# Kernel optimization log

Measured on AMD Instinct MI355X. Metric: run time of the kernel, lower is better.

Reference implementation:

```python
import jax, jax.numpy as jnp
import numpy as np

B, N, C = 8, 8192, 256
H = 8            # num_heads
D = C // H       # head dim = 32
P = 64           # proj_size (Linformer rank)


def setup_inputs() -> dict:
    key = jax.random.key(0)
    ks = jax.random.split(key, 12)
    s = lambda fan_in: 1.0 / np.sqrt(fan_in)
    return {
        "x": jax.random.normal(ks[0], (B, N, C), jnp.float32),
        "Wqkvv": jax.random.normal(ks[1], (4 * C, C), jnp.float32) * s(C),
        "WE": jax.random.normal(ks[2], (P, N), jnp.float32) * s(N),
        "bE": jax.random.normal(ks[3], (P,), jnp.float32) * s(N),
        "WF": jax.random.normal(ks[4], (P, N), jnp.float32) * s(N),
        "bF": jax.random.normal(ks[5], (P,), jnp.float32) * s(N),
        "Wo1": jax.random.normal(ks[6], (C // 2, C), jnp.float32) * s(C),
        "bo1": jax.random.normal(ks[7], (C // 2,), jnp.float32) * s(C),
        "Wo2": jax.random.normal(ks[8], (C // 2, C), jnp.float32) * s(C),
        "bo2": jax.random.normal(ks[9], (C // 2,), jnp.float32) * s(C),
        "temp1": jnp.ones((H, 1, 1), jnp.float32),
        "temp2": jnp.ones((H, 1, 1), jnp.float32),
    }


def _l2norm(v, axis=-1, eps=1e-12):
    # matches torch F.normalize
    n = jnp.sqrt(jnp.sum(v * v, axis=axis, keepdims=True))
    return v / jnp.maximum(n, eps)


def reference(x, Wqkvv, WE, bE, WF, bF, Wo1, bo1, Wo2, bo2, temp1, temp2):
    b, n, c = x.shape
    # qkvv: [b,n,4c] -> [4,b,h,d,n]  (includes the .transpose(-2,-1) of each part)
    qkvv = jnp.einsum('bnc,fc->bnf', x, Wqkvv).reshape(b, n, 4, H, D)
    qkvv = qkvv.transpose(2, 0, 3, 4, 1)
    q, k, v_ca, v_sa = qkvv[0], qkvv[1], qkvv[2], qkvv[3]  # each [b,h,d,n]

    # Linformer-style low-rank projections along the token axis
    k_proj = jnp.einsum('bhdn,pn->bhdp', k, WE) + bE   # [b,h,d,p]
    v_proj = jnp.einsum('bhdn,pn->bhdp', v_sa, WF) + bF

    qn = _l2norm(q)
    kn = _l2norm(k)

    # --- channel attention branch (XCiT-style) ---
    attn_ca = jnp.einsum('bhdn,bhen->bhde', qn, kn) * temp1[None]  # [b,h,d,d]
    attn_ca = jax.nn.softmax(attn_ca, axis=-1)  # dropout: eval mode (identity)
    x_ca = jnp.einsum('bhde,bhen->bhdn', attn_ca, v_ca)
    x_ca = x_ca.transpose(0, 3, 1, 2).reshape(b, n, c)  # [b,n,c]

    # --- spatial attention branch (low-rank) ---
    attn_sa = jnp.einsum('bhdn,bhdp->bhnp', qn, k_proj) * temp2[None]  # [b,h,n,p]
    attn_sa = jax.nn.softmax(attn_sa, axis=-1)
    x_sa = jnp.einsum('bhnp,bhdp->bhnd', attn_sa, v_proj)  # [b,h,n,d]
    # faithful to original: permute(0,3,1,2).reshape(b,n,c)
    x_sa = x_sa.transpose(0, 3, 1, 2).reshape(b, n, c)

    x_sa = jnp.einsum('bnc,oc->bno', x_sa, Wo1) + bo1
    x_ca = jnp.einsum('bnc,oc->bno', x_ca, Wo2) + bo2
    return jnp.concatenate((x_sa, x_ca), axis=-1)
```

## Files before the change

kernel.cpp:

```cpp
#include <hip/hip_runtime.h>
#include <hip/hip_bf16.h>
#include <stdint.h>


typedef __attribute__((ext_vector_type(8))) __bf16 bf16x8;
typedef __attribute__((ext_vector_type(4))) __bf16 bf16x4;
typedef __attribute__((ext_vector_type(4))) float f32x4;

#define MFMA(a, b, c) __builtin_amdgcn_mfma_f32_16x16x32_bf16((a), (b), (c), 0, 0, 0)

__device__ __forceinline__ void gl2lds16(const __bf16* g, __bf16* l) {
  __builtin_amdgcn_global_load_lds(
      (const __attribute__((address_space(1))) void*)(const void*)g,
      (__attribute__((address_space(3))) void*)(void*)l, 16, 0, 0);
}

__device__ __forceinline__ int detect_f32(const unsigned int* __restrict__ xw) {
  int c = 0;
#pragma unroll
  for (int i = 0; i < 64; ++i) {
    const unsigned int u = xw[i];
    c += (((u >> 7) & 0xFF) >= 0xC0) ? 1 : 0;
    c += (((u >> 23) & 0xFF) >= 0xC0) ? 1 : 0;
  }
  return c > 8;
}

__global__ __launch_bounds__(256) void k_convert_x(const void* __restrict__ src,
                                                   __bf16* __restrict__ dst) {
  const int i = (blockIdx.x * 256 + threadIdx.x) * 8;
  if (detect_f32((const unsigned int*)src)) {
    const float* s = (const float*)src;
    bf16x8 v;
#pragma unroll
    for (int j = 0; j < 8; ++j) v[j] = (__bf16)s[i + j];
    *(bf16x8*)(dst + i) = v;
  } else {
    *(bf16x8*)(dst + i) = *(const bf16x8*)((const __bf16*)src + i);
  }
}

__global__ __launch_bounds__(256) void k_convert_w(
    const void* s0, const void* s1, const void* s2, const void* s3, const void* s4,
    const void* s5, const void* s6, const void* s7, const void* s8, const void* s9,
    const void* s10, __bf16* __restrict__ cw, const void* __restrict__ xsrc) {
  const int i = (blockIdx.x * 256 + threadIdx.x) * 8;
  if (i >= 1376656) return;
  const void* s;
  int base;
  if (i < 262144)        { s = s0;  base = 0; }
  else if (i < 786432)   { s = s1;  base = 262144; }
  else if (i < 786496)   { s = s2;  base = 786432; }
  else if (i < 1310784)  { s = s3;  base = 786496; }
  else if (i < 1310848)  { s = s4;  base = 1310784; }
  else if (i < 1343616)  { s = s5;  base = 1310848; }
  else if (i < 1343744)  { s = s6;  base = 1343616; }
  else if (i < 1376512)  { s = s7;  base = 1343744; }
  else if (i < 1376640)  { s = s8;  base = 1376512; }
  else if (i < 1376648)  { s = s9;  base = 1376640; }
  else                   { s = s10; base = 1376648; }
  const int li = i - base;
  if (detect_f32((const unsigned int*)xsrc)) {
    const float* sf = (const float*)s;
#pragma unroll
    for (int j = 0; j < 8; ++j) cw[i + j] = (__bf16)sf[li + j];
  } else {
    const __bf16* sb = (const __bf16*)s;
#pragma unroll
    for (int j = 0; j < 8; ++j) cw[i + j] = sb[li + j];
  }
}

__global__ __launch_bounds__(256) void k_qkvv(const __bf16* __restrict__ x,
                                              const __bf16* __restrict__ Wq,
                                              __bf16* __restrict__ qkvv,
                                              float* __restrict__ npart) {
  __shared__ alignas(16) __bf16 As[2][128 * 32];
  __shared__ alignas(16) __bf16 Bs[2][128 * 32];
  __shared__ alignas(16) __bf16 Cs[32 * 136];
  const int t = threadIdx.x, lane = t & 63;
  const int wr = t >> 7, wc = (t >> 6) & 1;
  const int l15 = lane & 15, g = lane >> 4;
  const int f0 = blockIdx.y * 128;
  const int t0 = blockIdx.x * 128;
  f32x4 acc[4][4] = {};
  const int r = t >> 2;
  const int c8 = ((t & 3) ^ ((t >> 3) & 3)) * 8;
  const int cx = ((g ^ ((l15 >> 1) & 3)) * 8);
#pragma unroll
  for (int i = 0; i < 2; ++i) {
    gl2lds16(Wq + (size_t)(f0 + i * 64 + r) * 256 + c8, &As[0][i * 2048 + t * 8]);
    gl2lds16(x + (size_t)(t0 + i * 64 + r) * 256 + c8, &Bs[0][i * 2048 + t * 8]);
  }
  __syncthreads();
  for (int ks = 0; ks < 8; ++ks) {
    const int cur = ks & 1, nxt = cur ^ 1;
    if (ks < 7) {
      const int k1 = (ks + 1) * 32;
#pragma unroll
      for (int i = 0; i < 2; ++i) {
        gl2lds16(Wq + (size_t)(f0 + i * 64 + r) * 256 + k1 + c8, &As[nxt][i * 2048 + t * 8]);
        gl2lds16(x + (size_t)(t0 + i * 64 + r) * 256 + k1 + c8, &Bs[nxt][i * 2048 + t * 8]);
      }
    }
    bf16x8 af[4], bfr[4];
#pragma unroll
    for (int i = 0; i < 4; ++i) {
      af[i] = *(const bf16x8*)(&As[cur][(wr * 64 + i * 16 + l15) * 32 + cx]);
      bfr[i] = *(const bf16x8*)(&Bs[cur][(wc * 64 + i * 16 + l15) * 32 + cx]);
    }
#pragma unroll
    for (int i = 0; i < 4; ++i)
#pragma unroll
      for (int j = 0; j < 4; ++j) acc[i][j] = MFMA(af[i], bfr[j], acc[i][j]);
    __syncthreads();
  }
  const int b = t0 >> 13;
  const int n0 = t0 & 8191;
  for (int i = 0; i < 4; ++i) {
    if (i) __syncthreads();
#pragma unroll
    for (int j = 0; j < 4; ++j)
#pragma unroll
      for (int rr = 0; rr < 4; ++rr)
        Cs[(wr * 16 + g * 4 + rr) * 136 + wc * 64 + j * 16 + l15] = (__bf16)acc[i][j][rr];
    __syncthreads();
#pragma unroll
    for (int half = 0; half < 2; ++half) {
      const int row_l = (t >> 4) + half * 16;
      const int col8 = (t & 15) * 8;
      const bf16x8 v = *(const bf16x8*)(Cs + row_l * 136 + col8);
      const int f = f0 + (row_l >> 4) * 64 + i * 16 + (row_l & 15);
      *(bf16x8*)(qkvv + (size_t)(((f >> 8) * 8 + b) * 256 + (f & 255)) * 8192 + n0 + col8) = v;
      if (f0 < 512) {
        float s = 0.f;
#pragma unroll
        for (int jj = 0; jj < 8; ++jj) { const float q = (float)v[jj]; s += q * q; }
#pragma unroll
        for (int off = 1; off < 16; off <<= 1) s += __shfl_xor(s, off, 16);
        if ((t & 15) == 0) npart[(size_t)blockIdx.x * 512 + f] = s;
      }
    }
  }
}

__global__ __launch_bounds__(256) void k_nred(const float* __restrict__ npart,
                                              float* __restrict__ qsum,
                                              float* __restrict__ ksum) {
  const int which = blockIdx.x >> 3, b = blockIdx.x & 7;
  const int c = threadIdx.x;
  float s = 0.f;
#pragma unroll 4
  for (int j = 0; j < 64; ++j)
    s += npart[(size_t)(b * 64 + j) * 512 + which * 256 + c];
  (which ? ksum : qsum)[b * 256 + c] = s;
}

__global__ __launch_bounds__(256) void k_ef(const __bf16* __restrict__ x,
                                            const __bf16* __restrict__ WE,
                                            const __bf16* __restrict__ WF,
                                            float* __restrict__ pbufE) {
  __shared__ alignas(16) __bf16 Xs[32 * 264];
  const int t = threadIdx.x, lane = t & 63, w = t >> 6;
  const int l15 = lane & 15, g = lane >> 4;
  const int kc = blockIdx.x, b = blockIdx.y, pj = blockIdx.z;
  const __bf16* Wp = pj ? WF : WE;
  f32x4 acc[4][4] = {};
  const int sr = t >> 3, sc = (t & 7) * 8;
  for (int ks = 0; ks < 16; ++ks) {
    const int n0 = kc * 512 + ks * 32;
    __syncthreads();
#pragma unroll
    for (int q = 0; q < 4; ++q)
      *(bf16x8*)(&Xs[sr * 264 + q * 64 + sc]) =
          *(const bf16x8*)(x + (size_t)(b * 8192 + n0 + sr) * 256 + q * 64 + sc);
    __syncthreads();
    bf16x8 af[4];
#pragma unroll
    for (int i = 0; i < 4; ++i)
      af[i] = *(const bf16x8*)(Wp + (size_t)(i * 16 + l15) * 8192 + n0 + g * 8);
#pragma unroll
    for (int j = 0; j < 4; ++j) {
      union { bf16x8 v; unsigned short u[8]; } bq;
#pragma unroll
      for (int jj = 0; jj < 8; ++jj)
        bq.u[jj] = *(const unsigned short*)(&Xs[(g * 8 + jj) * 264 + w * 64 + j * 16 + l15]);
#pragma unroll
      for (int i = 0; i < 4; ++i) acc[i][j] = MFMA(af[i], bq.v, acc[i][j]);
    }
  }
  float* dst = pbufE + (size_t)((pj * 8 + b) * 16 + kc) * 16384;
#pragma unroll
  for (int i = 0; i < 4; ++i)
#pragma unroll
    for (int j = 0; j < 4; ++j)
#pragma unroll
      for (int rr = 0; rr < 4; ++rr)
        dst[(i * 16 + g * 4 + rr) * 256 + w * 64 + j * 16 + l15] = acc[i][j][rr];
}

__global__ __launch_bounds__(256) void k_zred(const float* __restrict__ pbufE,
                                              float* __restrict__ Z) {
  const int idx = blockIdx.x * 256 + threadIdx.x;
  const int grp = idx >> 14;
  const int pc = idx & 16383;
  const float* src = pbufE + (size_t)grp * 16 * 16384 + pc;
  float s = 0.f;
#pragma unroll
  for (int k = 0; k < 16; ++k) s += src[(size_t)k * 16384];
  Z[(size_t)grp * 16384 + pc] = s;
}

__global__ __launch_bounds__(256) void k_proj2(const float* __restrict__ Z,
                                               const __bf16* __restrict__ Wq,
                                               const __bf16* __restrict__ bE,
                                               const __bf16* __restrict__ bF,
                                               const float* __restrict__ qsum,
                                               const __bf16* __restrict__ t2,
                                               __bf16* __restrict__ kprojT,
                                               __bf16* __restrict__ vprojb) {
  __shared__ float Zs[8][260];
  const int bx = blockIdx.x;
  const int pj = bx >> 9, bh = (bx >> 3) & 63, pch = bx & 7;
  const int b = bh >> 3, h = bh & 7;
  const int t = threadIdx.x;
  {
    const int pr = t >> 5, c8 = (t & 31) * 8;
    const float* zr = Z + (size_t)((pj * 8 + b) * 64 + pch * 8 + pr) * 256 + c8;
    *(f32x4*)(&Zs[pr][c8]) = *(const f32x4*)(zr);
    *(f32x4*)(&Zs[pr][c8 + 4]) = *(const f32x4*)(zr + 4);
  }
  __syncthreads();
  const int pl = t >> 5, p = pch * 8 + pl, d = t & 31;
  const int f = (pj ? 768 : 256) + h * 32 + d;
  const __bf16* wr = Wq + (size_t)f * 256;
  float acc = 0.f;
#pragma unroll
  for (int c = 0; c < 256; c += 8) {
    const bf16x8 w8 = *(const bf16x8*)(wr + c);
#pragma unroll
    for (int jj = 0; jj < 8; ++jj) acc += (float)w8[jj] * Zs[pl][c + jj];
  }
  if (pj == 0) {
    const float qi = 1.0f / fmaxf(sqrtf(qsum[bh * 32 + d]), 1e-12f);
    kprojT[bh * 2048 + p * 32 + d] = (__bf16)((acc + (float)bE[p]) * qi * (float)t2[h]);
  } else {
    vprojb[bh * 2048 + d * 64 + p] = (__bf16)(acc + (float)bF[p]);
  }
}

__global__ __launch_bounds__(256) void k_sca_part(const __bf16* __restrict__ qkvv,
                                                  float* __restrict__ spart) {
  const int bh = blockIdx.x, kc = blockIdx.y;
  const int t = threadIdx.x, lane = t & 63, w = t >> 6;
  const __bf16* qb = qkvv + (size_t)(bh * 32) * 8192;
  const __bf16* kb = qkvv + (size_t)(2048 + bh * 32) * 8192;
  f32x4 acc[2][2] = {};
  const int kbase = kc * 1024 + w * 256 + (lane >> 4) * 8;
#pragma unroll
  for (int ks = 0; ks < 256; ks += 32) {
    bf16x8 af[2], bfr[2];
#pragma unroll
    for (int i = 0; i < 2; ++i) {
      af[i] = *(const bf16x8*)(qb + (size_t)(i * 16 + (lane & 15)) * 8192 + kbase + ks);
      bfr[i] = *(const bf16x8*)(kb + (size_t)(i * 16 + (lane & 15)) * 8192 + kbase + ks);
    }
#pragma unroll
    for (int i = 0; i < 2; ++i)
#pragma unroll
      for (int j = 0; j < 2; ++j) acc[i][j] = MFMA(af[i], bfr[j], acc[i][j]);
  }
  float* dst = spart + (size_t)((bh * 8 + kc) * 4 + w) * 1024;
#pragma unroll
  for (int i = 0; i < 2; ++i)
#pragma unroll
    for (int j = 0; j < 2; ++j)
#pragma unroll
      for (int rr = 0; rr < 4; ++rr)
        dst[(i * 16 + (lane >> 4) * 4 + rr) * 32 + j * 16 + (lane & 15)] = acc[i][j][rr];
}

__global__ __launch_bounds__(256) void k_sca_softmax(const float* __restrict__ spart,
                                                     const float* __restrict__ qsum,
                                                     const float* __restrict__ ksum,
                                                     const __bf16* __restrict__ temp1,
                                                     __bf16* __restrict__ attnb) {
  const int bh = blockIdx.x;
  __shared__ float S[1024];
  const int t = threadIdx.x;
  const float tmp = (float)temp1[bh & 7];
  for (int idx = t; idx < 1024; idx += 256) {
    float s = 0.f;
    const float* src = spart + (size_t)bh * 32768 + idx;
#pragma unroll
    for (int k = 0; k < 32; ++k) s += src[k * 1024];
    const float qi = 1.0f / fmaxf(sqrtf(qsum[bh * 32 + (idx >> 5)]), 1e-12f);
    const float ki = 1.0f / fmaxf(sqrtf(ksum[bh * 32 + (idx & 31)]), 1e-12f);
    S[idx] = s * qi * ki * tmp;
  }
  __syncthreads();
  const int lane = t & 63, w = t >> 6;
#pragma unroll
  for (int rr = 0; rr < 4; ++rr) {
    const int row = rr * 8 + w * 2 + (lane >> 5);
    const int e = lane & 31;
    float v = S[row * 32 + e];
    float m = v;
#pragma unroll
    for (int off = 16; off; off >>= 1) m = fmaxf(m, __shfl_xor(m, off, 32));
    const float ex = __expf(v - m);
    float sm = ex;
#pragma unroll
    for (int off = 16; off; off >>= 1) sm += __shfl_xor(sm, off, 32);
    attnb[(size_t)bh * 1024 + row * 32 + e] = (__bf16)(ex / sm);
  }
}

union alignas(16) CasaSmem {
  struct { __bf16 V[32 * 264]; __bf16 L[64 * 72]; } ca;
  struct { __bf16 Q[32 * 264]; __bf16 P[4][16 * 72]; __bf16 L[32 * 72]; } sa;
};

__global__ __launch_bounds__(256) void k_casa(const __bf16* __restrict__ qkvv,
                                              const __bf16* __restrict__ attnb,
                                              const __bf16* __restrict__ kprojT,
                                              const __bf16* __restrict__ vprojb,
                                              __bf16* __restrict__ xca,
                                              __bf16* __restrict__ xsa) {
  __shared__ CasaSmem sm;
  const int t = threadIdx.x, lane = t & 63, w = t >> 6;
  const int l15 = lane & 15, g = lane >> 4;
  if (blockIdx.y < 64) {
    const int bh = blockIdx.y, b = bh >> 3, h = bh & 7;
    const __bf16* vb = qkvv + (size_t)(4096 + bh * 32) * 8192;
    {
      const int er = t >> 5, nc8 = (t & 31) * 8;
#pragma unroll
      for (int l = 0; l < 4; ++l) {
        const int e = l * 8 + er;
        *(bf16x8*)(&sm.ca.V[e * 264 + nc8]) =
            *(const bf16x8*)(vb + (size_t)e * 8192 + blockIdx.x * 256 + nc8);
      }
    }
    bf16x8 aa[2];
#pragma unroll
    for (int mi = 0; mi < 2; ++mi)
      aa[mi] = *(const bf16x8*)(attnb + bh * 1024 + (mi * 16 + l15) * 32 + g * 8);
    __syncthreads();
#pragma unroll
    for (int it = 0; it < 4; ++it) {
      const int nl = it * 64 + w * 16 + l15;
      union { bf16x8 v; unsigned short u[8]; } bq;
#pragma unroll
      for (int j = 0; j < 8; ++j)
        bq.u[j] = *(const unsigned short*)(&sm.ca.V[(g * 8 + j) * 264 + nl]);
      f32x4 o[2] = {};
#pragma unroll
      for (int mi = 0; mi < 2; ++mi) o[mi] = MFMA(aa[mi], bq.v, o[mi]);
      if (it) __syncthreads();
#pragma unroll
      for (int mi = 0; mi < 2; ++mi) {
        bf16x4 p4;
#pragma unroll
        for (int rr = 0; rr < 4; ++rr) p4[rr] = (__bf16)o[mi][rr];
        *(bf16x4*)(&sm.ca.L[(w * 16 + l15) * 72 + mi * 16 + g * 4]) = p4;
      }
      __syncthreads();
      {
        const int row = t >> 2, ch = t & 3;
        const bf16x8 v = *(const bf16x8*)(&sm.ca.L[row * 72 + ch * 8]);
        *(bf16x8*)(xca + (size_t)(b * 8192 + blockIdx.x * 256 + it * 64 + row) * 256 +
                   h * 32 + ch * 8) = v;
      }
    }
  } else {
    const int bh = blockIdx.y - 64;
    const __bf16* qb = qkvv + (size_t)(bh * 32) * 8192;
    {
      const int er = t >> 5, nc8 = (t & 31) * 8;
#pragma unroll
      for (int l = 0; l < 4; ++l) {
        const int e = l * 8 + er;
        *(bf16x8*)(&sm.sa.Q[e * 264 + nc8]) =
            *(const bf16x8*)(qb + (size_t)e * 8192 + blockIdx.x * 256 + nc8);
      }
    }
    bf16x8 ka[4], va[2][2];
#pragma unroll
    for (int tile = 0; tile < 4; ++tile)
      ka[tile] = *(const bf16x8*)(kprojT + bh * 2048 + (tile * 16 + l15) * 32 + g * 8);
#pragma unroll
    for (int mi = 0; mi < 2; ++mi)
#pragma unroll
      for (int kh = 0; kh < 2; ++kh)
        va[mi][kh] = *(const bf16x8*)(vprojb + bh * 2048 + (mi * 16 + l15) * 64 + kh * 32 + g * 8);
    __syncthreads();
    __bf16* Pw = &sm.sa.P[w][0];
#pragma unroll
    for (int it = 0; it < 4; ++it) {
      const int nl = it * 64 + w * 16 + l15;
      union { bf16x8 v; unsigned short u[8]; } bq;
#pragma unroll
      for (int j = 0; j < 8; ++j)
        bq.u[j] = *(const unsigned short*)(&sm.sa.Q[(g * 8 + j) * 264 + nl]);
      f32x4 st[4];
#pragma unroll
      for (int tile = 0; tile < 4; ++tile) {
        f32x4 z = {};
        st[tile] = MFMA(ka[tile], bq.v, z);
      }
      float m = st[0][0];
#pragma unroll
      for (int tile = 0; tile < 4; ++tile)
#pragma unroll
        for (int rr = 0; rr < 4; ++rr) m = fmaxf(m, st[tile][rr]);
      m = fmaxf(m, __shfl_xor(m, 16, 64));
      m = fmaxf(m, __shfl_xor(m, 32, 64));
      float sum = 0.f;
#pragma unroll
      for (int tile = 0; tile < 4; ++tile) {
        bf16x4 p4;
#pragma unroll
        for (int rr = 0; rr < 4; ++rr) {
          const float ex = __expf(st[tile][rr] - m);
          sum += ex;
          p4[rr] = (__bf16)ex;
        }
        *(bf16x4*)(Pw + l15 * 72 + tile * 16 + g * 4) = p4;
      }
      sum += __shfl_xor(sum, 16, 64);
      sum += __shfl_xor(sum, 32, 64);
      const float inv = 1.0f / sum;
      f32x4 o[2] = {};
#pragma unroll
      for (int kh = 0; kh < 2; ++kh) {
        const bf16x8 pf = *(const bf16x8*)(Pw + l15 * 72 + kh * 32 + g * 8);
#pragma unroll
        for (int mi = 0; mi < 2; ++mi) o[mi] = MFMA(va[mi][kh], pf, o[mi]);
      }
      if (it) __syncthreads();
#pragma unroll
      for (int mi = 0; mi < 2; ++mi)
#pragma unroll
        for (int rr = 0; rr < 4; ++rr) {
          const int d = mi * 16 + g * 4 + rr;
          sm.sa.L[d * 72 + w * 16 + l15] = (__bf16)(o[mi][rr] * inv);
        }
      __syncthreads();
      {
        const int row = t >> 3, ch = t & 7;
        const bf16x8 v = *(const bf16x8*)(&sm.sa.L[row * 72 + ch * 8]);
        *(bf16x8*)(xsa + (size_t)(bh * 32 + row) * 8192 + blockIdx.x * 256 + it * 64 +
                   ch * 8) = v;
      }
    }
  }
}

__global__ __launch_bounds__(256) void k_out(const __bf16* __restrict__ xsa,
                                             const __bf16* __restrict__ xca,
                                             const __bf16* __restrict__ Wo1,
                                             const __bf16* __restrict__ bo1,
                                             const __bf16* __restrict__ Wo2,
                                             const __bf16* __restrict__ bo2,
                                             void* __restrict__ outv,
                                             const void* __restrict__ xsrc) {
  __shared__ alignas(16) __bf16 As[2][128 * 32];
  __shared__ alignas(16) __bf16 Bs[2][128 * 32];
  const int t = threadIdx.x, lane = t & 63;
  const int wr = t >> 7, wc = (t >> 6) & 1;
  const int l15 = lane & 15, g = lane >> 4;
  const int nt = blockIdx.x, b = blockIdx.y, br = blockIdx.z;
  const int isf32 = detect_f32((const unsigned int*)xsrc);
  const __bf16* Wo = br ? Wo2 : Wo1;
  const __bf16* bo = br ? bo2 : bo1;
  f32x4 acc[4][4] = {};
  const int r = t >> 2;
  const int c8 = ((t & 3) ^ ((t >> 3) & 3)) * 8;
  const int cx = ((g ^ ((l15 >> 1) & 3)) * 8);
  const int row_b = nt * 128 + r;
  auto asrc = [&](int i, int k0) -> const __bf16* {
    const int row = row_b + i * 64;
    if (br == 0)
      return xsa + (size_t)((b * 8 + ((row >> 5) & 7)) * 32 + (row >> 8)) * 8192 +
             (row & 31) * 256 + k0 + c8;
    return xca + (size_t)(b * 8192 + row) * 256 + k0 + c8;
  };
#pragma unroll
  for (int i = 0; i < 2; ++i) {
    gl2lds16(asrc(i, 0), &As[0][i * 2048 + t * 8]);
    gl2lds16(Wo + (size_t)(i * 64 + r) * 256 + c8, &Bs[0][i * 2048 + t * 8]);
  }
  __syncthreads();
  for (int ks = 0; ks < 8; ++ks) {
    const int cur = ks & 1, nxt = cur ^ 1;
    if (ks < 7) {
      const int k1 = (ks + 1) * 32;
#pragma unroll
      for (int i = 0; i < 2; ++i) {
        gl2lds16(asrc(i, k1), &As[nxt][i * 2048 + t * 8]);
        gl2lds16(Wo + (size_t)(i * 64 + r) * 256 + k1 + c8, &Bs[nxt][i * 2048 + t * 8]);
      }
    }
    bf16x8 af[4], bfr[4];
#pragma unroll
    for (int i = 0; i < 4; ++i) {
      af[i] = *(const bf16x8*)(&As[cur][(wr * 64 + i * 16 + l15) * 32 + cx]);
      bfr[i] = *(const bf16x8*)(&Bs[cur][(wc * 64 + i * 16 + l15) * 32 + cx]);
    }
#pragma unroll
    for (int i = 0; i < 4; ++i)
#pragma unroll
      for (int j = 0; j < 4; ++j) acc[i][j] = MFMA(af[i], bfr[j], acc[i][j]);
    __syncthreads();
  }
  float bias[4];
#pragma unroll
  for (int j = 0; j < 4; ++j) bias[j] = (float)bo[wc * 64 + j * 16 + l15];
#pragma unroll
  for (int i = 0; i < 4; ++i) {
#pragma unroll
    for (int j = 0; j < 4; ++j) {
      const int col = wc * 64 + j * 16 + l15;
#pragma unroll
      for (int rr = 0; rr < 4; ++rr) {
        const int row = nt * 128 + wr * 64 + i * 16 + g * 4 + rr;
        const float val = acc[i][j][rr] + bias[j];
        const size_t oi = (size_t)(b * 8192 + row) * 256 + br * 128 + col;
        if (isf32) ((float*)outv)[oi] = val;
        else ((__bf16*)outv)[oi] = (__bf16)val;
      }
    }
  }
}

extern "C" void kernel_launch(void* const* d_in, const int* in_sizes, int n_in,
                              void* d_out, int out_size, void* d_ws, size_t ws_size,
                              hipStream_t stream) {
  char* ws = (char*)d_ws;
  __bf16* qkvv   = (__bf16*)(ws);
  __bf16* cinx   = (__bf16*)(ws + 134217728ull);
  __bf16* xca    = (__bf16*)(ws + 134217728ull);
  float*  pbufE  = (float*)(ws + 167772160ull);
  float*  npart  = (float*)(ws + 184549376ull);
  float*  Zb     = (float*)(ws + 185597952ull);
  float*  spart  = (float*)(ws + 184549376ull);
  __bf16* xsa    = (__bf16*)(ws + 167772160ull);
  __bf16* kprojT = (__bf16*)(ws + 201326592ull);
  __bf16* vprojb = (__bf16*)(ws + 201588736ull);
  float*  qsum   = (float*)(ws + 201850880ull);
  float*  ksum   = (float*)(ws + 201859072ull);
  __bf16* attnb  = (__bf16*)(ws + 201867264ull);
  __bf16* cw     = (__bf16*)(ws + 201998336ull);

  __bf16* cWq  = cw;
  __bf16* cWE  = cw + 262144;
  __bf16* cbE  = cw + 786432;
  __bf16* cWF  = cw + 786496;
  __bf16* cbF  = cw + 1310784;
  __bf16* cWo1 = cw + 1310848;
  __bf16* cbo1 = cw + 1343616;
  __bf16* cWo2 = cw + 1343744;
  __bf16* cbo2 = cw + 1376512;
  __bf16* ct1  = cw + 1376640;
  __bf16* ct2  = cw + 1376648;

  k_convert_x<<<8192, 256, 0, stream>>>(d_in[0], cinx);
  k_convert_w<<<673, 256, 0, stream>>>(d_in[1], d_in[2], d_in[3], d_in[4], d_in[5],
                                       d_in[6], d_in[7], d_in[8], d_in[9], d_in[10],
                                       d_in[11], cw, d_in[0]);
  k_qkvv<<<dim3(512, 6), 256, 0, stream>>>(cinx, cWq, qkvv, npart);
  k_nred<<<16, 256, 0, stream>>>(npart, qsum, ksum);
  k_ef<<<dim3(16, 8, 2), 256, 0, stream>>>(cinx, cWE, cWF, pbufE);
  k_zred<<<1024, 256, 0, stream>>>(pbufE, Zb);
  k_proj2<<<1024, 256, 0, stream>>>(Zb, cWq, cbE, cbF, qsum, ct2, kprojT, vprojb);
  k_sca_part<<<dim3(64, 8), 256, 0, stream>>>(qkvv, spart);
  k_sca_softmax<<<dim3(64), 256, 0, stream>>>(spart, qsum, ksum, ct1, attnb);
  k_casa<<<dim3(32, 128), 256, 0, stream>>>(qkvv, attnb, kprojT, vprojb, xca, xsa);
  k_out<<<dim3(64, 8, 2), 256, 0, stream>>>(xsa, xca, cWo1, cbo1, cWo2, cbo2, d_out, d_in[0]);
}
```

Measured before the change: 329.6 us.

## Double-buffer k_ef X tiles with async LDS loads and double its split-K

k_ef now stages X tiles into LDS with async global-to-LDS loads, double-buffered so the next tile loads while MFMAs run on the current one. An XOR swizzle replaces the padded LDS layout to avoid bank conflicts. The token axis is split into 32 chunks instead of 16, giving twice as many blocks to fill the device. In exchange the partial-sum buffer doubles, so k_zred reads twice as much. That buffer moves into workspace space after the three stored q/k/v_ca slices.

```diff
diff --git a/kernel.cpp b/kernel.cpp
--- a/kernel.cpp
+++ b/kernel.cpp
@@ -160,36 +160,49 @@
                                             const __bf16* __restrict__ WE,
                                             const __bf16* __restrict__ WF,
                                             float* __restrict__ pbufE) {
-  __shared__ alignas(16) __bf16 Xs[32 * 264];
+  __shared__ alignas(16) __bf16 Xs[2][32 * 256];
   const int t = threadIdx.x, lane = t & 63, w = t >> 6;
   const int l15 = lane & 15, g = lane >> 4;
-  const int kc = blockIdx.x, b = blockIdx.y, pj = blockIdx.z;
+  const int kc = blockIdx.x;
+  const int pj = blockIdx.y & 1, b = blockIdx.y >> 1;
   const __bf16* Wp = pj ? WF : WE;
+  const __bf16* xb = x + (size_t)b * 8192 * 256;
   f32x4 acc[4][4] = {};
-  const int sr = t >> 3, sc = (t & 7) * 8;
-  for (int ks = 0; ks < 16; ++ks) {
-    const int n0 = kc * 512 + ks * 32;
-    __syncthreads();
-#pragma unroll
-    for (int q = 0; q < 4; ++q)
-      *(bf16x8*)(&Xs[sr * 264 + q * 64 + sc]) =
-          *(const bf16x8*)(x + (size_t)(b * 8192 + n0 + sr) * 256 + q * 64 + sc);
-    __syncthreads();
+  const int kb = kc * 256;
+  const int srow2 = w * 2 + (lane >> 5);
+  const int slot = lane & 31;
+  auto stage = [&](int n0, __bf16* buf) {
+#pragma unroll
+    for (int q = 0; q < 4; ++q) {
+      const int row = q * 8 + srow2;
+      const int c16 = slot ^ ((row >> 3) & 3);
+      gl2lds16(xb + (size_t)(n0 + row) * 256 + c16 * 8, buf + row * 256 + slot * 8);
+    }
+  };
+  stage(kb, Xs[0]);
+  __syncthreads();
+  for (int ks = 0; ks < 8; ++ks) {
+    const int cur = ks & 1, nxt = cur ^ 1;
+    if (ks < 7) stage(kb + (ks + 1) * 32, Xs[nxt]);
+    const int n0 = kb + ks * 32;
     bf16x8 af[4];
 #pragma unroll
     for (int i = 0; i < 4; ++i)
       af[i] = *(const bf16x8*)(Wp + (size_t)(i * 16 + l15) * 8192 + n0 + g * 8);
 #pragma unroll
     for (int j = 0; j < 4; ++j) {
+      const int c = w * 64 + j * 16 + l15;
+      const int cb = (((c >> 3) ^ g) * 8) | (c & 7);
       union { bf16x8 v; unsigned short u[8]; } bq;
 #pragma unroll
       for (int jj = 0; jj < 8; ++jj)
-        bq.u[jj] = *(const unsigned short*)(&Xs[(g * 8 + jj) * 264 + w * 64 + j * 16 + l15]);
+        bq.u[jj] = *(const unsigned short*)(&Xs[cur][(g * 8 + jj) * 256 + cb]);
 #pragma unroll
       for (int i = 0; i < 4; ++i) acc[i][j] = MFMA(af[i], bq.v, acc[i][j]);
     }
-  }
-  float* dst = pbufE + (size_t)((pj * 8 + b) * 16 + kc) * 16384;
+    __syncthreads();
+  }
+  float* dst = pbufE + (size_t)((pj * 8 + b) * 32 + kc) * 16384;
 #pragma unroll
   for (int i = 0; i < 4; ++i)
 #pragma unroll
@@ -204,10 +217,10 @@
   const int idx = blockIdx.x * 256 + threadIdx.x;
   const int grp = idx >> 14;
   const int pc = idx & 16383;
-  const float* src = pbufE + (size_t)grp * 16 * 16384 + pc;
+  const float* src = pbufE + (size_t)grp * 32 * 16384 + pc;
   float s = 0.f;
 #pragma unroll
-  for (int k = 0; k < 16; ++k) s += src[(size_t)k * 16384];
+  for (int k = 0; k < 32; ++k) s += src[(size_t)k * 16384];
   Z[(size_t)grp * 16384 + pc] = s;
 }
 
@@ -539,9 +552,9 @@
                               hipStream_t stream) {
   char* ws = (char*)d_ws;
   __bf16* qkvv   = (__bf16*)(ws);
+  float*  pbufE  = (float*)(ws + 100663296ull);
   __bf16* cinx   = (__bf16*)(ws + 134217728ull);
   __bf16* xca    = (__bf16*)(ws + 134217728ull);
-  float*  pbufE  = (float*)(ws + 167772160ull);
   float*  npart  = (float*)(ws + 184549376ull);
   float*  Zb     = (float*)(ws + 185597952ull);
   float*  spart  = (float*)(ws + 184549376ull);
@@ -571,7 +584,7 @@
                                        d_in[11], cw, d_in[0]);
   k_qkvv<<<dim3(512, 6), 256, 0, stream>>>(cinx, cWq, qkvv, npart);
   k_nred<<<16, 256, 0, stream>>>(npart, qsum, ksum);
-  k_ef<<<dim3(16, 8, 2), 256, 0, stream>>>(cinx, cWE, cWF, pbufE);
+  k_ef<<<dim3(32, 16), 256, 0, stream>>>(cinx, cWE, cWF, pbufE);
   k_zred<<<1024, 256, 0, stream>>>(pbufE, Zb);
   k_proj2<<<1024, 256, 0, stream>>>(Zb, cWq, cbE, cbF, qsum, ct2, kprojT, vprojb);
   k_sca_part<<<dim3(64, 8), 256, 0, stream>>>(qkvv, spart);
```

Result: faster. 314.1 us (-4.7%).
